# Optimization experiments

Hardware: AMD Instinct MI355X
Metric: run time of the kernel (lower is better)

The kernel has to match this reference:

```python
import jax, jax.numpy as jnp
import numpy as np

N_NODES = 100000
N_EDGES = 1600000
FEAT = 512
CLS = 64
HID = 200  # each hop layer output width; 3 hops -> 600 concat


def spmm(row, col, vals, x):
    # out[r] = sum_{e: row[e]==r} vals[e] * x[col[e]]  -- sparse A @ x
    return jax.ops.segment_sum(x[col] * vals[:, None], row, num_segments=x.shape[0])


def setup_inputs() -> dict:
    key = jax.random.key(0)
    ks = jax.random.split(key, 12)
    adj_index = jax.random.randint(ks[0], (2, N_EDGES), 0, N_NODES, dtype=jnp.int64)
    # scale like a normalized adjacency (~1/avg_degree) to keep powers stable
    adj_values = jax.random.uniform(ks[1], (N_EDGES,), dtype=jnp.float32) * (1.0 / 16.0)
    features = jax.random.normal(ks[2], (N_NODES, FEAT), dtype=jnp.float32)
    s1 = (2.0 / (FEAT + HID)) ** 0.5
    s2 = (2.0 / (3 * HID + HID)) ** 0.5
    sf = (2.0 / (3 * HID + CLS)) ** 0.5
    W1 = jax.random.normal(ks[3], (3, FEAT, HID), dtype=jnp.float32) * s1
    b1 = jax.random.normal(ks[4], (3, HID), dtype=jnp.float32) * 0.01
    W2 = jax.random.normal(ks[5], (3, 3 * HID, HID), dtype=jnp.float32) * s2
    b2 = jax.random.normal(ks[6], (3, HID), dtype=jnp.float32) * 0.01
    Wfc = jax.random.normal(ks[7], (3 * HID, CLS), dtype=jnp.float32) * sf
    bfc = jax.random.normal(ks[8], (CLS,), dtype=jnp.float32) * 0.01
    return {"adj_index": adj_index, "adj_values": adj_values, "features": features,
            "W1": W1, "b1": b1, "W2": W2, "b2": b2, "Wfc": Wfc, "bfc": bfc}


def reference(adj_index, adj_values, features, W1, b1, W2, b2, Wfc, bfc):
    # Inference mode: dropout is identity.
    row, col = adj_index[0], adj_index[1]
    # upper (sparse) layers: linear + bias + relu, then (iterations-1) spmm hops
    outs1 = []
    for i in range(3):  # iterations = i + 1
        h = jax.nn.relu(features @ W1[i] + b1[i][None, :])
        for _ in range(i):
            h = spmm(row, col, adj_values, h)
        outs1.append(h)
    abstract1 = jnp.concatenate(outs1, axis=1)  # [N, 600]
    # bottom (dense) layers: linear, (iterations-1) spmm hops, then + bias
    outs2 = []
    for i in range(3):
        h = abstract1 @ W2[i]
        for _ in range(i):
            h = spmm(row, col, adj_values, h)
        h = h + b2[i][None, :]
        outs2.append(h)
    abstract2 = jnp.concatenate(outs2, axis=1)  # [N, 600]
    node_emb = abstract2 @ Wfc + bfc  # [N, CLS]
    predictions = jax.nn.log_softmax(node_emb, axis=1)
    return node_emb, predictions
```

## Files before the change

kernel.cpp:

```cpp
#include <hip/hip_runtime.h>

typedef unsigned short u16;
typedef unsigned int u32;
typedef __attribute__((ext_vector_type(8))) short short8;
typedef __attribute__((ext_vector_type(4))) float f32x4;
typedef __attribute__((ext_vector_type(4))) u32 u32x4;
typedef __attribute__((ext_vector_type(2))) u32 u32x2;

#define NN 100000
#define PAD 640

__device__ __forceinline__ float b2f(u16 u) {
    union { u32 i; float f; } v; v.i = ((u32)u) << 16; return v.f;
}
__device__ __forceinline__ u16 f2b(float f) {
    union { float f; u32 i; } v; v.f = f;
    u32 x = v.i;
    return (u16)((x + 0x7FFFu + ((x >> 16) & 1u)) >> 16);
}
__device__ __forceinline__ u32 pack2(float lo, float hi) {
    return (u32)f2b(lo) | ((u32)f2b(hi) << 16);
}
__device__ __forceinline__ float rdf(const void* p, size_t i, int f) {
    return f ? ((const float*)p)[i] : b2f(((const u16*)p)[i]);
}
__device__ __forceinline__ void gload16(const u16* g, u16* l) {
    __builtin_amdgcn_global_load_lds(
        (const __attribute__((address_space(1))) void*)g,
        (__attribute__((address_space(3))) void*)l, 16, 0, 0);
}

__global__ void probe_k(const int* __restrict__ idx,
                        const void* avals, const void* feats, const void* W1,
                        const void* b1, const void* W2, const void* b2,
                        const void* Wfc, const void* bfc,
                        int* __restrict__ flags) {
    if (threadIdx.x != 0 || blockIdx.x != 0) return;
    int z = 1;
    for (int i = 0; i < 128; ++i)
        if (idx[2 * i + 1] != 0) { z = 0; break; }
    flags[0] = z;
    const void* ts[8] = {avals, feats, W1, b1, W2, b2, Wfc, bfc};
    const int ns[8] = {256, 256, 256, 128, 256, 128, 256, 32};
    for (int t = 0; t < 8; ++t) {
        const u16* p = (const u16*)ts[t];
        int n = ns[t], bad = 0;
        for (int i = 0; i < n; ++i) {
            int e = (p[2 * i] >> 7) & 0xFF;
            if (e >= 133) bad++;
        }
        flags[1 + t] = (bad * 8 >= n) ? 1 : 0;
    }
}

__device__ __forceinline__ int load_row(const int* idx, int E, int f, int e) {
    return f ? idx[2 * e] : idx[e];
}
__device__ __forceinline__ int load_col(const int* idx, int E, int f, int e) {
    return f ? idx[2 * E + 2 * e] : idx[E + e];
}

__global__ void featconv_k(const void* __restrict__ src, u16* __restrict__ dst,
                           const int* __restrict__ flags) {
    int i = blockIdx.x * 256 + threadIdx.x;
    if (i >= NN * 512) return;
    int f = flags[2];
    dst[i] = f ? f2b(((const float*)src)[i]) : ((const u16*)src)[i];
}
__global__ void w1t_k(const void* __restrict__ W1, u16* __restrict__ w1t,
                      const int* __restrict__ flags) {
    int i = blockIdx.x * 256 + threadIdx.x;
    if (i >= 640 * 512) return;
    int n = i >> 9, k = i & 511;
    float v = 0.f;
    if (n < 600) {
        int ib = n / 200, c = n % 200;
        v = rdf(W1, (size_t)ib * 102400 + (size_t)k * 200 + c, flags[3]);
    }
    w1t[i] = f2b(v);
}
__global__ void w2t_k(const void* __restrict__ W2, u16* __restrict__ w2t,
                      const int* __restrict__ flags) {
    int i = blockIdx.x * 256 + threadIdx.x;
    if (i >= 640 * 640) return;
    int n = i / 640, k = i % 640;
    float v = 0.f;
    if (n < 600 && k < 600) {
        int ib = n / 200, c = n % 200;
        v = rdf(W2, (size_t)ib * 120000 + (size_t)k * 200 + c, flags[5]);
    }
    w2t[i] = f2b(v);
}
__global__ void wfct_k(const void* __restrict__ Wfc, u16* __restrict__ wfct,
                       const int* __restrict__ flags) {
    int i = blockIdx.x * 256 + threadIdx.x;
    if (i >= 64 * 640) return;
    int n = i / 640, k = i % 640;
    float v = 0.f;
    if (k < 600) v = rdf(Wfc, (size_t)k * 64 + n, flags[7]);
    wfct[i] = f2b(v);
}
__global__ void bconv_k(const void* __restrict__ b1, const void* __restrict__ b2,
                        const void* __restrict__ bfc, float* __restrict__ o,
                        const int* __restrict__ flags) {
    int i = blockIdx.x * 256 + threadIdx.x;
    if (i < 600) o[i] = rdf(b1, i, flags[4]);
    else if (i < 1200) o[i] = rdf(b2, i - 600, flags[6]);
    else if (i < 1264) o[i] = rdf(bfc, i - 1200, flags[8]);
}

__global__ void count_k(const int* __restrict__ idx, int E, const int* __restrict__ flags,
                        int* __restrict__ counts) {
    int e = blockIdx.x * 256 + threadIdx.x;
    if (e >= E) return;
    int r = load_row(idx, E, flags[0], e);
    if ((u32)r >= NN) return;
    atomicAdd(&counts[r], 1);
}

__global__ void chunksum_k(const int* __restrict__ counts, int* __restrict__ chsum) {
    __shared__ int sm[256];
    int c = blockIdx.x, t = threadIdx.x;
    int base = c * 1024, s = 0;
    for (int i = t; i < 1024; i += 256) {
        int g = base + i;
        if (g < NN) s += counts[g];
    }
    sm[t] = s; __syncthreads();
    for (int off = 128; off; off >>= 1) {
        if (t < off) sm[t] += sm[t + off];
        __syncthreads();
    }
    if (t == 0) chsum[c] = sm[0];
}

__global__ void chscan_k(const int* __restrict__ chsum, int nch, int* __restrict__ choff,
                         int* __restrict__ row_ptr, int E) {
    if (threadIdx.x == 0 && blockIdx.x == 0) {
        int run = 0;
        for (int c = 0; c < nch; ++c) { choff[c] = run; run += chsum[c]; }
        row_ptr[NN] = run;
    }
}

__global__ __launch_bounds__(1024) void scan_k(const int* __restrict__ counts,
                                               const int* __restrict__ choff,
                                               int* __restrict__ row_ptr,
                                               int* __restrict__ cursor) {
    __shared__ int sm[1024];
    int c = blockIdx.x, t = threadIdx.x;
    int g = c * 1024 + t;
    int v = (g < NN) ? counts[g] : 0;
    sm[t] = v;
    __syncthreads();
    for (int off = 1; off < 1024; off <<= 1) {
        int add = (t >= off) ? sm[t - off] : 0;
        __syncthreads();
        sm[t] += add;
        __syncthreads();
    }
    if (g < NN) {
        int ex = choff[c] + sm[t] - v;
        row_ptr[g] = ex;
        cursor[g] = ex;
    }
}

__global__ void scatter_k(const int* __restrict__ idx, const void* __restrict__ avals, int E,
                          const int* __restrict__ flags, int* __restrict__ cursor,
                          int* __restrict__ colsS, float* __restrict__ valsS) {
    int e = blockIdx.x * 256 + threadIdx.x;
    if (e >= E) return;
    int f = flags[0];
    int r = load_row(idx, E, f, e);
    if ((u32)r >= NN) return;
    int c = load_col(idx, E, f, e);
    if ((u32)c >= NN) c = 0;
    int p = atomicAdd(&cursor[r], 1);
    colsS[p] = c;
    valsS[p] = rdf(avals, e, flags[1]);
}

__global__ __launch_bounds__(256) void gemm128_k(
    const u16* __restrict__ A, const u16* __restrict__ Bt,
    u16* __restrict__ C, float* __restrict__ Cf,
    const float* __restrict__ bias, int bias_n, int relu,
    int M, int K, int lda, int ldc) {
    __shared__ u16 As[128 * 32];
    __shared__ u16 Bs[128 * 32];
    const int tid = threadIdx.x;
    const int wave = tid >> 6, lane = tid & 63;
    const int bm = blockIdx.x * 128, bn = blockIdx.y * 128;
    const int wrow = (wave >> 1) * 64, wcol = (wave & 1) * 64;
    const int l15 = lane & 15, l4 = lane >> 4;
    f32x4 acc[4][4] = {};

    const int c0 = wave * 2;
    const int rowA0 = c0 * 16 + (lane >> 2);
    const int rowA1 = rowA0 + 16;
    const int colE = (lane & 3) * 8;
    int gr0 = bm + rowA0; if (gr0 >= M) gr0 = M - 1;
    int gr1 = bm + rowA1; if (gr1 >= M) gr1 = M - 1;
    const u16* a0p = A + (size_t)gr0 * lda + colE;
    const u16* a1p = A + (size_t)gr1 * lda + colE;
    const u16* b0p = Bt + (size_t)(bn + rowA0) * K + colE;
    const u16* b1p = Bt + (size_t)(bn + rowA1) * K + colE;
    u16* lA0 = As + c0 * 512;
    u16* lA1 = As + c0 * 512 + 512;
    u16* lB0 = Bs + c0 * 512;
    u16* lB1 = Bs + c0 * 512 + 512;

    for (int k0 = 0; k0 < K; k0 += 32) {
        __syncthreads();
        gload16(a0p + k0, lA0);
        gload16(a1p + k0, lA1);
        gload16(b0p + k0, lB0);
        gload16(b1p + k0, lB1);
        __syncthreads();
        short8 af[4], bf[4];
#pragma unroll
        for (int t = 0; t < 4; ++t) {
            af[t] = *(const short8*)&As[(wrow + t * 16 + l15) * 32 + l4 * 8];
            bf[t] = *(const short8*)&Bs[(wcol + t * 16 + l15) * 32 + l4 * 8];
        }
#pragma unroll
        for (int mi = 0; mi < 4; ++mi)
#pragma unroll
            for (int ni = 0; ni < 4; ++ni)
                acc[mi][ni] = __builtin_amdgcn_mfma_f32_16x16x32_bf16(
                    af[mi], bf[ni], acc[mi][ni], 0, 0, 0);
    }

#pragma unroll
    for (int mi = 0; mi < 4; ++mi)
#pragma unroll
        for (int ni = 0; ni < 4; ++ni)
#pragma unroll
            for (int r4 = 0; r4 < 4; ++r4) {
                int row = bm + wrow + mi * 16 + l4 * 4 + r4;
                int col = bn + wcol + ni * 16 + l15;
                if (row < M) {
                    float v = acc[mi][ni][r4];
                    if (bias && col < bias_n) v += bias[col];
                    if (relu) v = fmaxf(v, 0.0f);
                    if (C) C[(size_t)row * ldc + col] = f2b(v);
                    if (Cf) Cf[(size_t)row * ldc + col] = v;
                }
            }
}

__global__ __launch_bounds__(256) void gemm_k(
    const u16* __restrict__ A, const u16* __restrict__ Bt,
    u16* __restrict__ C, float* __restrict__ Cf,
    const float* __restrict__ bias, int bias_n, int relu,
    int M, int K, int lda, int ldc) {
    __shared__ u16 As[64][40];
    __shared__ u16 Bs[64][40];
    const int tid = threadIdx.x;
    const int wave = tid >> 6, lane = tid & 63;
    const int bm = blockIdx.x * 64, bn = blockIdx.y * 64;
    const int wr = (wave >> 1) * 32, wc = (wave & 1) * 32;
    const int l15 = lane & 15, l4 = lane >> 4;
    f32x4 acc[2][2] = {};

    const int srow = tid >> 2;
    const int skoff = (tid & 3) * 8;
    const bool arow_ok = (bm + srow) < M;
    const u16* aptr = A + (size_t)(bm + srow) * lda + skoff;
    const u16* bptr = Bt + (size_t)(bn + srow) * K + skoff;

    for (int k0 = 0; k0 < K; k0 += 32) {
        short8 av = {};
        if (arow_ok) av = *(const short8*)(aptr + k0);
        short8 bv = *(const short8*)(bptr + k0);
        __syncthreads();
        *(short8*)&As[srow][skoff] = av;
        *(short8*)&Bs[srow][skoff] = bv;
        __syncthreads();
        short8 a0 = *(const short8*)&As[wr + l15][l4 * 8];
        short8 a1 = *(const short8*)&As[wr + 16 + l15][l4 * 8];
        short8 bb0 = *(const short8*)&Bs[wc + l15][l4 * 8];
        short8 bb1 = *(const short8*)&Bs[wc + 16 + l15][l4 * 8];
        acc[0][0] = __builtin_amdgcn_mfma_f32_16x16x32_bf16(a0, bb0, acc[0][0], 0, 0, 0);
        acc[0][1] = __builtin_amdgcn_mfma_f32_16x16x32_bf16(a0, bb1, acc[0][1], 0, 0, 0);
        acc[1][0] = __builtin_amdgcn_mfma_f32_16x16x32_bf16(a1, bb0, acc[1][0], 0, 0, 0);
        acc[1][1] = __builtin_amdgcn_mfma_f32_16x16x32_bf16(a1, bb1, acc[1][1], 0, 0, 0);
    }

#pragma unroll
    for (int mi = 0; mi < 2; ++mi)
#pragma unroll
        for (int ni = 0; ni < 2; ++ni)
#pragma unroll
            for (int r = 0; r < 4; ++r) {
                int row = bm + wr + mi * 16 + l4 * 4 + r;
                int col = bn + wc + ni * 16 + l15;
                if (row < M) {
                    float v = acc[mi][ni][r];
                    if (bias && col < bias_n) v += bias[col];
                    if (relu) v = fmaxf(v, 0.0f);
                    if (C) C[(size_t)row * ldc + col] = f2b(v);
                    if (Cf) Cf[(size_t)row * ldc + col] = v;
                }
            }
}

__global__ __launch_bounds__(256) void spmm400_k(
    const int* __restrict__ row_ptr, const int* __restrict__ cols,
    const float* __restrict__ vals, int E,
    const u16* __restrict__ X, u16* __restrict__ Y1, u16* __restrict__ Yt,
    const float* __restrict__ bias1) {
    int r = blockIdx.x * 4 + (threadIdx.x >> 6);
    if (r >= NN) return;
    int lane = threadIdx.x & 63;
    int s = row_ptr[r], e = row_ptr[r + 1];
    if (e > E) e = E;
    if (s < 0) s = 0;
    if (s > e) s = e;
    float a[8] = {0.f, 0.f, 0.f, 0.f, 0.f, 0.f, 0.f, 0.f};
    const bool act = lane < 50;
    const u32* xb = (const u32*)X;
    int i = s;
    for (; i + 2 <= e; i += 2) {
        int ca = cols[i]; if ((u32)ca >= NN) ca = 0;
        int cb = cols[i + 1]; if ((u32)cb >= NN) cb = 0;
        float va = vals[i], vb = vals[i + 1];
        if (act) {
            u32x4 ga = *(const u32x4*)(xb + (size_t)ca * 320 + lane * 4);
            u32x4 gb = *(const u32x4*)(xb + (size_t)cb * 320 + lane * 4);
#pragma unroll
            for (int q = 0; q < 4; ++q) {
                union { u32 i; float f; } lo, hi;
                lo.i = ga[q] << 16; hi.i = ga[q] & 0xffff0000u;
                a[2 * q] = fmaf(va, lo.f, a[2 * q]);
                a[2 * q + 1] = fmaf(va, hi.f, a[2 * q + 1]);
                lo.i = gb[q] << 16; hi.i = gb[q] & 0xffff0000u;
                a[2 * q] = fmaf(vb, lo.f, a[2 * q]);
                a[2 * q + 1] = fmaf(vb, hi.f, a[2 * q + 1]);
            }
        }
    }
    if (i < e) {
        int ca = cols[i]; if ((u32)ca >= NN) ca = 0;
        float va = vals[i];
        if (act) {
            u32x4 ga = *(const u32x4*)(xb + (size_t)ca * 320 + lane * 4);
#pragma unroll
            for (int q = 0; q < 4; ++q) {
                union { u32 i; float f; } lo, hi;
                lo.i = ga[q] << 16; hi.i = ga[q] & 0xffff0000u;
                a[2 * q] = fmaf(va, lo.f, a[2 * q]);
                a[2 * q + 1] = fmaf(va, hi.f, a[2 * q + 1]);
            }
        }
    }
    if (bias1 && lane < 25) {
#pragma unroll
        for (int q = 0; q < 8; ++q) a[q] += bias1[lane * 8 + q];
    }
    u32x4 o;
    o[0] = pack2(a[0], a[1]); o[1] = pack2(a[2], a[3]);
    o[2] = pack2(a[4], a[5]); o[3] = pack2(a[6], a[7]);
    if (lane < 25) {
        *(u32x4*)((u32*)Y1 + (size_t)r * 320 + lane * 4) = o;
    } else if (lane < 50) {
        *(u32x4*)((u32*)Yt + (size_t)r * 100 + (lane - 25) * 4) = o;
    }
}

__global__ __launch_bounds__(256) void spmm200_k(
    const int* __restrict__ row_ptr, const int* __restrict__ cols,
    const float* __restrict__ vals, int E,
    const u16* __restrict__ X, int ldx,
    u16* __restrict__ Y, int ldy,
    const float* __restrict__ bias) {
    int r = blockIdx.x * 4 + (threadIdx.x >> 6);
    if (r >= NN) return;
    int lane = threadIdx.x & 63;
    int s = row_ptr[r], e = row_ptr[r + 1];
    if (e > E) e = E;
    if (s < 0) s = 0;
    if (s > e) s = e;
    float a[4] = {0.f, 0.f, 0.f, 0.f};
    const bool act = lane < 50;
    const int ldxw = ldx >> 1, ldyw = ldy >> 1;
    const u32* xb = (const u32*)X;
    int i = s;
    for (; i + 2 <= e; i += 2) {
        int ca = cols[i]; if ((u32)ca >= NN) ca = 0;
        int cb = cols[i + 1]; if ((u32)cb >= NN) cb = 0;
        float va = vals[i], vb = vals[i + 1];
        if (act) {
            u32x2 ga = *(const u32x2*)(xb + (size_t)ca * ldxw + lane * 2);
            u32x2 gb = *(const u32x2*)(xb + (size_t)cb * ldxw + lane * 2);
#pragma unroll
            for (int q = 0; q < 2; ++q) {
                union { u32 i; float f; } lo, hi;
                lo.i = ga[q] << 16; hi.i = ga[q] & 0xffff0000u;
                a[2 * q] = fmaf(va, lo.f, a[2 * q]);
                a[2 * q + 1] = fmaf(va, hi.f, a[2 * q + 1]);
                lo.i = gb[q] << 16; hi.i = gb[q] & 0xffff0000u;
                a[2 * q] = fmaf(vb, lo.f, a[2 * q]);
                a[2 * q + 1] = fmaf(vb, hi.f, a[2 * q + 1]);
            }
        }
    }
    if (i < e) {
        int ca = cols[i]; if ((u32)ca >= NN) ca = 0;
        float va = vals[i];
        if (act) {
            u32x2 ga = *(const u32x2*)(xb + (size_t)ca * ldxw + lane * 2);
#pragma unroll
            for (int q = 0; q < 2; ++q) {
                union { u32 i; float f; } lo, hi;
                lo.i = ga[q] << 16; hi.i = ga[q] & 0xffff0000u;
                a[2 * q] = fmaf(va, lo.f, a[2 * q]);
                a[2 * q + 1] = fmaf(va, hi.f, a[2 * q + 1]);
            }
        }
    }
    if (bias && act) {
#pragma unroll
        for (int q = 0; q < 4; ++q) a[q] += bias[lane * 4 + q];
    }
    if (act) {
        u32x2 o;
        o[0] = pack2(a[0], a[1]); o[1] = pack2(a[2], a[3]);
        *(u32x2*)((u32*)Y + (size_t)r * ldyw + lane * 2) = o;
    }
}

__global__ void copyblk_k(const u16* __restrict__ src, u16* __restrict__ dst) {
    int i = blockIdx.x * 256 + threadIdx.x;
    if (i >= NN * 100) return;
    int r = i / 100, c = i % 100;
    ((u32*)dst)[(size_t)r * 320 + c] = ((const u32*)src)[(size_t)r * 320 + c];
}
__global__ void zeropad_k(u16* __restrict__ dst) {
    int i = blockIdx.x * 256 + threadIdx.x;
    if (i >= NN * 20) return;
    int r = i / 20, c = i % 20;
    ((u32*)dst)[(size_t)r * 320 + 300 + c] = 0u;
}
__global__ void copybias_k(const u16* __restrict__ src, u16* __restrict__ dst,
                           const float* __restrict__ bias) {
    int i = blockIdx.x * 256 + threadIdx.x;
    if (i >= NN * 200) return;
    int r = i / 200, c = i % 200;
    dst[(size_t)r * 640 + c] = f2b(b2f(src[(size_t)r * 640 + c]) + bias[c]);
}

__global__ void softmax_k(const float* __restrict__ ne, float* __restrict__ out) {
    int r = blockIdx.x * 4 + (threadIdx.x >> 6);
    if (r >= NN) return;
    int lane = threadIdx.x & 63;
    float v = ne[(size_t)r * 64 + lane];
    float m = v;
    for (int off = 32; off; off >>= 1) m = fmaxf(m, __shfl_xor(m, off, 64));
    float e = expf(v - m);
    float ssum = e;
    for (int off = 32; off; off >>= 1) ssum += __shfl_xor(ssum, off, 64);
    out[(size_t)r * 64 + lane] = v - m - logf(ssum);
}

extern "C" void kernel_launch(void* const* d_in, const int* in_sizes, int n_in,
                              void* d_out, int out_size, void* d_ws, size_t ws_size,
                              hipStream_t stream) {
    const int* adj_idx = (const int*)d_in[0];
    const void* adj_vals = d_in[1];
    const void* feats = d_in[2];
    const void* W1 = d_in[3];
    const void* b1 = d_in[4];
    const void* W2 = d_in[5];
    const void* b2 = d_in[6];
    const void* Wfc = d_in[7];
    const void* bfc = d_in[8];
    const int E = in_sizes[1];
    (void)n_in; (void)out_size; (void)ws_size;

    char* ws = (char*)d_ws;
    size_t off = 0;
    auto alloc = [&](size_t b) { size_t o = off; off += (b + 255) & ~(size_t)255; return o; };
    u16* buf0 = (u16*)(ws + alloc((size_t)NN * PAD * 2));
    u16* buf1 = (u16*)(ws + alloc((size_t)NN * PAD * 2));
    u16* hop = (u16*)(ws + alloc((size_t)NN * 200 * 2));
    u16* w1t = (u16*)(ws + alloc((size_t)640 * 512 * 2));
    u16* w2t = (u16*)(ws + alloc((size_t)640 * 640 * 2));
    u16* wfct = (u16*)(ws + alloc((size_t)64 * 640 * 2));
    float* biasf = (float*)(ws + alloc(1264 * 4));
    int* counts = (int*)(ws + alloc((size_t)NN * 4));
    int* cursor = (int*)(ws + alloc((size_t)NN * 4));
    int* row_ptr = (int*)(ws + alloc((size_t)(NN + 1) * 4));
    int* chsum = (int*)(ws + alloc(4096));
    int* choff = (int*)(ws + alloc(4096));
    int* flags = (int*)(ws + alloc(256));
    int* colsS = (int*)(ws + alloc((size_t)E * 4));
    float* valsS = (float*)(ws + alloc((size_t)E * 4));

    u16* featsB = buf1;
    float* out_ne = (float*)d_out;
    float* out_pred = out_ne + (size_t)NN * 64;

    probe_k<<<1, 64, 0, stream>>>(adj_idx, adj_vals, feats, W1, b1, W2, b2, Wfc, bfc, flags);
    featconv_k<<<(NN * 512 + 255) / 256, 256, 0, stream>>>(feats, featsB, flags);
    w1t_k<<<(640 * 512 + 255) / 256, 256, 0, stream>>>(W1, w1t, flags);
    w2t_k<<<(640 * 640 + 255) / 256, 256, 0, stream>>>(W2, w2t, flags);
    wfct_k<<<(64 * 640 + 255) / 256, 256, 0, stream>>>(Wfc, wfct, flags);
    bconv_k<<<5, 256, 0, stream>>>(b1, b2, bfc, biasf, flags);

    hipMemsetAsync(counts, 0, NN * 4, stream);
    count_k<<<(E + 255) / 256, 256, 0, stream>>>(adj_idx, E, flags, counts);
    const int NCH = (NN + 1023) / 1024;
    chunksum_k<<<NCH, 256, 0, stream>>>(counts, chsum);
    chscan_k<<<1, 64, 0, stream>>>(chsum, NCH, choff, row_ptr, E);
    scan_k<<<NCH, 1024, 0, stream>>>(counts, choff, row_ptr, cursor);
    scatter_k<<<(E + 255) / 256, 256, 0, stream>>>(adj_idx, adj_vals, E, flags, cursor, colsS, valsS);

    dim3 g128((NN + 127) / 128, PAD / 128);
    gemm128_k<<<g128, 256, 0, stream>>>(featsB, w1t, buf0, nullptr, biasf, 600, 1, NN, 512, 512, PAD);
    copyblk_k<<<(NN * 100 + 255) / 256, 256, 0, stream>>>(buf0, buf1);
    zeropad_k<<<(NN * 20 + 255) / 256, 256, 0, stream>>>(buf1);
    spmm400_k<<<(NN + 3) / 4, 256, 0, stream>>>(row_ptr, colsS, valsS, E,
                                                buf0 + 200, buf1 + 200, hop, nullptr);
    spmm200_k<<<(NN + 3) / 4, 256, 0, stream>>>(row_ptr, colsS, valsS, E,
                                                hop, 200, buf1 + 400, PAD, nullptr);
    gemm128_k<<<g128, 256, 0, stream>>>(buf1, w2t, buf0, nullptr, nullptr, 0, 0, NN, PAD, PAD, PAD);
    copybias_k<<<(NN * 200 + 255) / 256, 256, 0, stream>>>(buf0, buf1, biasf + 600);
    spmm400_k<<<(NN + 3) / 4, 256, 0, stream>>>(row_ptr, colsS, valsS, E,
                                                buf0 + 200, buf1 + 200, hop, biasf + 800);
    spmm200_k<<<(NN + 3) / 4, 256, 0, stream>>>(row_ptr, colsS, valsS, E,
                                                hop, 200, buf1 + 400, PAD, biasf + 1000);
    dim3 gC((NN + 63) / 64, 1);
    gemm_k<<<gC, 256, 0, stream>>>(buf1, wfct, nullptr, out_ne, biasf + 1200, 64, 0, NN, PAD, PAD, 64);
    softmax_k<<<(NN + 3) / 4, 256, 0, stream>>>(out_ne, out_pred);
}
```

Before: 1.734 ms.

## Pad CSR rows to multiples of 8 with interleaved col/val, unroll SpMM gathers

Row segments in the CSR are now padded to a multiple of 8 edges, with zero-valued padding entries written by a new fill kernel. Columns and values are interleaved into one array so each 16-byte load brings two edges. The SpMM kernels issue 8 independent gathers per iteration with no tail loop, which increases memory-level parallelism. Feature conversion is also vectorized to 8 elements per thread. The cost is extra padding work and memory traffic on low-degree rows (average degree is 16, so padding can add up to 7 edges per row) and more registers per thread.

```diff
diff --git a/kernel.cpp b/kernel.cpp
--- a/kernel.cpp
+++ b/kernel.cpp
@@ -63,9 +63,23 @@
 __global__ void featconv_k(const void* __restrict__ src, u16* __restrict__ dst,
                            const int* __restrict__ flags) {
     int i = blockIdx.x * 256 + threadIdx.x;
-    if (i >= NN * 512) return;
+    if (i >= NN * 64) return;
     int f = flags[2];
-    dst[i] = f ? f2b(((const float*)src)[i]) : ((const u16*)src)[i];
+    size_t b = (size_t)i * 8;
+    short8 o;
+    if (f) {
+        const float* sf = (const float*)src + b;
+        f32x4 x0 = *(const f32x4*)sf;
+        f32x4 x1 = *(const f32x4*)(sf + 4);
+#pragma unroll
+        for (int q = 0; q < 4; ++q) {
+            o[q] = (short)f2b(x0[q]);
+            o[q + 4] = (short)f2b(x1[q]);
+        }
+    } else {
+        o = *(const short8*)((const u16*)src + b);
+    }
+    *(short8*)(dst + b) = o;
 }
 __global__ void w1t_k(const void* __restrict__ W1, u16* __restrict__ w1t,
                       const int* __restrict__ flags) {
@@ -108,6 +122,8 @@
     else if (i < 1200) o[i] = rdf(b2, i - 600, flags[6]);
     else if (i < 1264) o[i] = rdf(bfc, i - 1200, flags[8]);
 }
+
+__device__ __forceinline__ int pad8(int c) { return (c + 7) & ~7; }
 
 __global__ void count_k(const int* __restrict__ idx, int E, const int* __restrict__ flags,
                         int* __restrict__ counts) {
@@ -124,7 +140,7 @@
     int base = c * 1024, s = 0;
     for (int i = t; i < 1024; i += 256) {
         int g = base + i;
-        if (g < NN) s += counts[g];
+        if (g < NN) s += pad8(counts[g]);
     }
     sm[t] = s; __syncthreads();
     for (int off = 128; off; off >>= 1) {
@@ -150,7 +166,7 @@
     __shared__ int sm[1024];
     int c = blockIdx.x, t = threadIdx.x;
     int g = c * 1024 + t;
-    int v = (g < NN) ? counts[g] : 0;
+    int v = (g < NN) ? pad8(counts[g]) : 0;
     sm[t] = v;
     __syncthreads();
     for (int off = 1; off < 1024; off <<= 1) {
@@ -168,7 +184,7 @@
 
 __global__ void scatter_k(const int* __restrict__ idx, const void* __restrict__ avals, int E,
                           const int* __restrict__ flags, int* __restrict__ cursor,
-                          int* __restrict__ colsS, float* __restrict__ valsS) {
+                          int* __restrict__ edges) {
     int e = blockIdx.x * 256 + threadIdx.x;
     if (e >= E) return;
     int f = flags[0];
@@ -177,8 +193,19 @@
     int c = load_col(idx, E, f, e);
     if ((u32)c >= NN) c = 0;
     int p = atomicAdd(&cursor[r], 1);
-    colsS[p] = c;
-    valsS[p] = rdf(avals, e, flags[1]);
+    edges[2 * p] = c;
+    ((float*)edges)[2 * p + 1] = rdf(avals, e, flags[1]);
+}
+
+__global__ void padfill_k(const int* __restrict__ cursor, const int* __restrict__ row_ptr,
+                          int* __restrict__ edges) {
+    int r = blockIdx.x * 256 + threadIdx.x;
+    if (r >= NN) return;
+    int p = cursor[r], e = row_ptr[r + 1];
+    for (; p < e; ++p) {
+        edges[2 * p] = 0;
+        ((float*)edges)[2 * p + 1] = 0.f;
+    }
 }
 
 __global__ __launch_bounds__(256) void gemm128_k(
@@ -306,51 +333,45 @@
 }
 
 __global__ __launch_bounds__(256) void spmm400_k(
-    const int* __restrict__ row_ptr, const int* __restrict__ cols,
-    const float* __restrict__ vals, int E,
+    const int* __restrict__ row_ptr, const int* __restrict__ edges,
     const u16* __restrict__ X, u16* __restrict__ Y1, u16* __restrict__ Yt,
     const float* __restrict__ bias1) {
     int r = blockIdx.x * 4 + (threadIdx.x >> 6);
     if (r >= NN) return;
     int lane = threadIdx.x & 63;
     int s = row_ptr[r], e = row_ptr[r + 1];
-    if (e > E) e = E;
     if (s < 0) s = 0;
-    if (s > e) s = e;
+    if (e < s) e = s;
     float a[8] = {0.f, 0.f, 0.f, 0.f, 0.f, 0.f, 0.f, 0.f};
     const bool act = lane < 50;
-    const u32* xb = (const u32*)X;
-    int i = s;
-    for (; i + 2 <= e; i += 2) {
-        int ca = cols[i]; if ((u32)ca >= NN) ca = 0;
-        int cb = cols[i + 1]; if ((u32)cb >= NN) cb = 0;
-        float va = vals[i], vb = vals[i + 1];
+    const u32* xl = (const u32*)X + lane * 4;
+    for (int i = s; i < e; i += 8) {
+        int cc[8]; float vv[8];
+#pragma unroll
+        for (int j = 0; j < 4; ++j) {
+            u32x4 p = *(const u32x4*)(edges + 2 * (size_t)(i + 2 * j));
+            union { u32 u; float f; } w0, w1;
+            cc[2 * j] = (int)p[0];     w0.u = p[1];
+            cc[2 * j + 1] = (int)p[2]; w1.u = p[3];
+            vv[2 * j] = w0.f; vv[2 * j + 1] = w1.f;
+        }
         if (act) {
-            u32x4 ga = *(const u32x4*)(xb + (size_t)ca * 320 + lane * 4);
-            u32x4 gb = *(const u32x4*)(xb + (size_t)cb * 320 + lane * 4);
-#pragma unroll
-            for (int q = 0; q < 4; ++q) {
-                union { u32 i; float f; } lo, hi;
-                lo.i = ga[q] << 16; hi.i = ga[q] & 0xffff0000u;
-                a[2 * q] = fmaf(va, lo.f, a[2 * q]);
-                a[2 * q + 1] = fmaf(va, hi.f, a[2 * q + 1]);
-                lo.i = gb[q] << 16; hi.i = gb[q] & 0xffff0000u;
-                a[2 * q] = fmaf(vb, lo.f, a[2 * q]);
-                a[2 * q + 1] = fmaf(vb, hi.f, a[2 * q + 1]);
+            u32x4 g[8];
+#pragma unroll
+            for (int j = 0; j < 8; ++j) {
+                u32 c = (u32)cc[j]; if (c >= NN) c = 0;
+                g[j] = *(const u32x4*)(xl + (size_t)c * 320);
             }
-        }
-    }
-    if (i < e) {
-        int ca = cols[i]; if ((u32)ca >= NN) ca = 0;
-        float va = vals[i];
-        if (act) {
-            u32x4 ga = *(const u32x4*)(xb + (size_t)ca * 320 + lane * 4);
-#pragma unroll
-            for (int q = 0; q < 4; ++q) {
-                union { u32 i; float f; } lo, hi;
-                lo.i = ga[q] << 16; hi.i = ga[q] & 0xffff0000u;
-                a[2 * q] = fmaf(va, lo.f, a[2 * q]);
-                a[2 * q + 1] = fmaf(va, hi.f, a[2 * q + 1]);
+#pragma unroll
+            for (int j = 0; j < 8; ++j) {
+                float v = vv[j];
+#pragma unroll
+                for (int q = 0; q < 4; ++q) {
+                    union { u32 i; float f; } lo, hi;
+                    lo.i = g[j][q] << 16; hi.i = g[j][q] & 0xffff0000u;
+                    a[2 * q] = fmaf(v, lo.f, a[2 * q]);
+                    a[2 * q + 1] = fmaf(v, hi.f, a[2 * q + 1]);
+                }
             }
         }
     }
@@ -369,8 +390,7 @@
 }
 
 __global__ __launch_bounds__(256) void spmm200_k(
-    const int* __restrict__ row_ptr, const int* __restrict__ cols,
-    const float* __restrict__ vals, int E,
+    const int* __restrict__ row_ptr, const int* __restrict__ edges,
     const u16* __restrict__ X, int ldx,
     u16* __restrict__ Y, int ldy,
     const float* __restrict__ bias) {
@@ -378,44 +398,39 @@
     if (r >= NN) return;
     int lane = threadIdx.x & 63;
     int s = row_ptr[r], e = row_ptr[r + 1];
-    if (e > E) e = E;
     if (s < 0) s = 0;
-    if (s > e) s = e;
+    if (e < s) e = s;
     float a[4] = {0.f, 0.f, 0.f, 0.f};
     const bool act = lane < 50;
     const int ldxw = ldx >> 1, ldyw = ldy >> 1;
-    const u32* xb = (const u32*)X;
-    int i = s;
-    for (; i + 2 <= e; i += 2) {
-        int ca = cols[i]; if ((u32)ca >= NN) ca = 0;
-        int cb = cols[i + 1]; if ((u32)cb >= NN) cb = 0;
-        float va = vals[i], vb = vals[i + 1];
+    const u32* xl = (const u32*)X + lane * 2;
+    for (int i = s; i < e; i += 8) {
+        int cc[8]; float vv[8];
+#pragma unroll
+        for (int j = 0; j < 4; ++j) {
+            u32x4 p = *(const u32x4*)(edges + 2 * (size_t)(i + 2 * j));
+            union { u32 u; float f; } w0, w1;
+            cc[2 * j] = (int)p[0];     w0.u = p[1];
+            cc[2 * j + 1] = (int)p[2]; w1.u = p[3];
+            vv[2 * j] = w0.f; vv[2 * j + 1] = w1.f;
+        }
         if (act) {
-            u32x2 ga = *(const u32x2*)(xb + (size_t)ca * ldxw + lane * 2);
-            u32x2 gb = *(const u32x2*)(xb + (size_t)cb * ldxw + lane * 2);
-#pragma unroll
-            for (int q = 0; q < 2; ++q) {
-                union { u32 i; float f; } lo, hi;
-                lo.i = ga[q] << 16; hi.i = ga[q] & 0xffff0000u;
-                a[2 * q] = fmaf(va, lo.f, a[2 * q]);
-                a[2 * q + 1] = fmaf(va, hi.f, a[2 * q + 1]);
-                lo.i = gb[q] << 16; hi.i = gb[q] & 0xffff0000u;
-                a[2 * q] = fmaf(vb, lo.f, a[2 * q]);
-                a[2 * q + 1] = fmaf(vb, hi.f, a[2 * q + 1]);
+            u32x2 g[8];
+#pragma unroll
+            for (int j = 0; j < 8; ++j) {
+                u32 c = (u32)cc[j]; if (c >= NN) c = 0;
+                g[j] = *(const u32x2*)(xl + (size_t)c * ldxw);
             }
-        }
-    }
-    if (i < e) {
-        int ca = cols[i]; if ((u32)ca >= NN) ca = 0;
-        float va = vals[i];
-        if (act) {
-            u32x2 ga = *(const u32x2*)(xb + (size_t)ca * ldxw + lane * 2);
-#pragma unroll
-            for (int q = 0; q < 2; ++q) {
-                union { u32 i; float f; } lo, hi;
-                lo.i = ga[q] << 16; hi.i = ga[q] & 0xffff0000u;
-                a[2 * q] = fmaf(va, lo.f, a[2 * q]);
-                a[2 * q + 1] = fmaf(va, hi.f, a[2 * q + 1]);
+#pragma unroll
+            for (int j = 0; j < 8; ++j) {
+                float v = vv[j];
+#pragma unroll
+                for (int q = 0; q < 2; ++q) {
+                    union { u32 i; float f; } lo, hi;
+                    lo.i = g[j][q] << 16; hi.i = g[j][q] & 0xffff0000u;
+                    a[2 * q] = fmaf(v, lo.f, a[2 * q]);
+                    a[2 * q + 1] = fmaf(v, hi.f, a[2 * q + 1]);
+                }
             }
         }
     }
@@ -494,15 +509,14 @@
     int* chsum = (int*)(ws + alloc(4096));
     int* choff = (int*)(ws + alloc(4096));
     int* flags = (int*)(ws + alloc(256));
-    int* colsS = (int*)(ws + alloc((size_t)E * 4));
-    float* valsS = (float*)(ws + alloc((size_t)E * 4));
+    int* edgesS = (int*)(ws + alloc(((size_t)E + 8 * (size_t)NN) * 8));
 
     u16* featsB = buf1;
     float* out_ne = (float*)d_out;
     float* out_pred = out_ne + (size_t)NN * 64;
 
     probe_k<<<1, 64, 0, stream>>>(adj_idx, adj_vals, feats, W1, b1, W2, b2, Wfc, bfc, flags);
-    featconv_k<<<(NN * 512 + 255) / 256, 256, 0, stream>>>(feats, featsB, flags);
+    featconv_k<<<(NN * 64 + 255) / 256, 256, 0, stream>>>(feats, featsB, flags);
     w1t_k<<<(640 * 512 + 255) / 256, 256, 0, stream>>>(W1, w1t, flags);
     w2t_k<<<(640 * 640 + 255) / 256, 256, 0, stream>>>(W2, w2t, flags);
     wfct_k<<<(64 * 640 + 255) / 256, 256, 0, stream>>>(Wfc, wfct, flags);
@@ -514,21 +528,22 @@
     chunksum_k<<<NCH, 256, 0, stream>>>(counts, chsum);
     chscan_k<<<1, 64, 0, stream>>>(chsum, NCH, choff, row_ptr, E);
     scan_k<<<NCH, 1024, 0, stream>>>(counts, choff, row_ptr, cursor);
-    scatter_k<<<(E + 255) / 256, 256, 0, stream>>>(adj_idx, adj_vals, E, flags, cursor, colsS, valsS);
+    scatter_k<<<(E + 255) / 256, 256, 0, stream>>>(adj_idx, adj_vals, E, flags, cursor, edgesS);
+    padfill_k<<<(NN + 255) / 256, 256, 0, stream>>>(cursor, row_ptr, edgesS);
 
     dim3 g128((NN + 127) / 128, PAD / 128);
     gemm128_k<<<g128, 256, 0, stream>>>(featsB, w1t, buf0, nullptr, biasf, 600, 1, NN, 512, 512, PAD);
     copyblk_k<<<(NN * 100 + 255) / 256, 256, 0, stream>>>(buf0, buf1);
     zeropad_k<<<(NN * 20 + 255) / 256, 256, 0, stream>>>(buf1);
-    spmm400_k<<<(NN + 3) / 4, 256, 0, stream>>>(row_ptr, colsS, valsS, E,
+    spmm400_k<<<(NN + 3) / 4, 256, 0, stream>>>(row_ptr, edgesS,
                                                 buf0 + 200, buf1 + 200, hop, nullptr);
-    spmm200_k<<<(NN + 3) / 4, 256, 0, stream>>>(row_ptr, colsS, valsS, E,
+    spmm200_k<<<(NN + 3) / 4, 256, 0, stream>>>(row_ptr, edgesS,
                                                 hop, 200, buf1 + 400, PAD, nullptr);
     gemm128_k<<<g128, 256, 0, stream>>>(buf1, w2t, buf0, nullptr, nullptr, 0, 0, NN, PAD, PAD, PAD);
     copybias_k<<<(NN * 200 + 255) / 256, 256, 0, stream>>>(buf0, buf1, biasf + 600);
-    spmm400_k<<<(NN + 3) / 4, 256, 0, stream>>>(row_ptr, colsS, valsS, E,
+    spmm400_k<<<(NN + 3) / 4, 256, 0, stream>>>(row_ptr, edgesS,
                                                 buf0 + 200, buf1 + 200, hop, biasf + 800);
-    spmm200_k<<<(NN + 3) / 4, 256, 0, stream>>>(row_ptr, colsS, valsS, E,
+    spmm200_k<<<(NN + 3) / 4, 256, 0, stream>>>(row_ptr, edgesS,
                                                 hop, 200, buf1 + 400, PAD, biasf + 1000);
     dim3 gC((NN + 63) / 64, 1);
     gemm_k<<<gC, 256, 0, stream>>>(buf1, wfct, nullptr, out_ne, biasf + 1200, 64, 0, NN, PAD, PAD, 64);
```

New measurement: 1.664 ms. 1.04x faster.
